# Performance work log

Hardware: AMD Instinct MI355X
Metric: run time of the kernel (lower is better)

## Reference

```python
import jax, jax.numpy as jnp
import numpy as np

NUM_HEADS = 8


def setup_inputs() -> dict:
    key = jax.random.key(0)
    k1, k2, k3 = jax.random.split(key, 3)
    B, C, D, H, W = 2, 512, 32, 32, 32
    x = jax.random.normal(k1, (B, C, D, H, W), dtype=jnp.float32)
    w_qkv = jax.random.normal(k2, (3 * C, C), dtype=jnp.float32) * 0.02
    b_qkv = jnp.zeros((3 * C,), dtype=jnp.float32)
    w_out = jax.random.normal(k3, (C, C), dtype=jnp.float32) * 0.02
    b_out = jnp.zeros((C,), dtype=jnp.float32)
    return {"x": x, "w_qkv": w_qkv, "b_qkv": b_qkv, "w_out": w_out, "b_out": b_out}


def reference(x, w_qkv, b_qkv, w_out, b_out):
    B, C, D, H, W = x.shape
    nh = NUM_HEADS
    hd = C // nh
    # 1x1x1 conv3d == pointwise linear over channel dim
    qkv = jnp.einsum('bcdhw,oc->bodhw', x, w_qkv) + b_qkv[None, :, None, None, None]
    q, k, v = jnp.split(qkv, 3, axis=1)  # each [B,C,D,H,W]

    def to_heads(t):
        # [B,C,D,H,W] -> [B,nh,hd,D,H,W] -> [B,H,W,nh,D,hd]
        return t.reshape(B, nh, hd, D, H, W).transpose(0, 4, 5, 1, 3, 2)

    q, k, v = to_heads(q), to_heads(k), to_heads(v)
    scale = hd ** -0.5
    # attention along the depth axis D: attn [B,H,W,nh,D,D]
    attn = jnp.einsum('bhwnic,bhwnjc->bhwnij', q, k) * scale
    attn = jax.nn.softmax(attn, axis=-1)
    out = jnp.einsum('bhwnij,bhwnjc->bhwnic', attn, v)  # [B,H,W,nh,D,hd]
    # [B,H,W,nh,D,hd] -> [B,nh,hd,D,H,W] -> [B,C,D,H,W]
    out = out.transpose(0, 3, 5, 4, 1, 2).reshape(B, C, D, H, W)
    out = jnp.einsum('bcdhw,oc->bodhw', out, w_out) + b_out[None, :, None, None, None]
    return out + x
```

## Files before the change

kernel.cpp:

```cpp
#include <hip/hip_runtime.h>


typedef __bf16 bf16x8 __attribute__((ext_vector_type(8)));
typedef float  f32x4  __attribute__((ext_vector_type(4)));
typedef float  f32x16 __attribute__((ext_vector_type(16)));

__device__ __forceinline__ float b2f(unsigned int u) {
    union { float f; unsigned int i; } x; x.i = u << 16; return x.f;
}
__device__ __forceinline__ unsigned short f2b(float f) {
    union { float f; unsigned int i; } x; x.f = f;
    unsigned int r = x.i + 0x7FFFu + ((x.i >> 16) & 1u);
    return (unsigned short)(r >> 16);
}
__device__ __forceinline__ unsigned int cvtpk(float lo, float hi) {
    unsigned int r;
    asm("v_cvt_pk_bf16_f32 %0, %1, %2" : "=v"(r) : "v"(lo), "v"(hi));
    return r;
}
__device__ __forceinline__ f32x4 mfma16(bf16x8 a, bf16x8 b, f32x4 c) {
    return __builtin_amdgcn_mfma_f32_16x16x32_bf16(a, b, c, 0, 0, 0);
}
__device__ __forceinline__ f32x16 mfma32(bf16x8 a, bf16x8 b, f32x16 c) {
    return __builtin_amdgcn_mfma_f32_32x32x16_bf16(a, b, c, 0, 0, 0);
}
__device__ __forceinline__ void gload16(const void* g, void* l) {
    __builtin_amdgcn_global_load_lds((const unsigned int*)g, (unsigned int*)l, 16, 0, 0);
}

__global__ __launch_bounds__(256) void xprep(const float* __restrict__ x,
                                             const float* __restrict__ wq_f,
                                             const float* __restrict__ wo_f,
                                             unsigned short* __restrict__ xT,
                                             unsigned short* __restrict__ wbf) {
    const int bid = blockIdx.x;
    const int t   = threadIdx.x;
    if (bid >= 2048) {
        int i0 = (bid - 2048) * 1024 + t;
        #pragma unroll
        for (int k = 0; k < 4; ++k) {
            int i = i0 + k * 256;
            const float* src;
            int off;
            if (i < 196608) { src = wq_f; off = i * 4; }
            else            { src = wo_f; off = (i - 196608) * 4; }
            float4 v = *(const float4*)(src + off);
            *(uint2*)(wbf + (size_t)i * 4) = make_uint2(cvtpk(v.x, v.y), cvtpk(v.z, v.w));
        }
        return;
    }
    __shared__ __align__(16) char tile[32768];
    const int c0 = (bid & 7) * 64;
    const int s0 = (bid >> 3) * 256;
    const int b  = s0 >> 15;
    const int sp = s0 & 32767;

    const float* px = x + (size_t)b * 16777216 + (size_t)(c0 + (t & 7) * 8) * 32768 + sp + (t >> 3) * 8;
    float va[8][8];
    #pragma unroll
    for (int j = 0; j < 8; ++j) {
        float4 a0 = *(const float4*)(px + (size_t)j * 32768);
        float4 a1 = *(const float4*)(px + (size_t)j * 32768 + 4);
        va[j][0] = a0.x; va[j][1] = a0.y; va[j][2] = a0.z; va[j][3] = a0.w;
        va[j][4] = a1.x; va[j][5] = a1.y; va[j][6] = a1.z; va[j][7] = a1.w;
    }
    #pragma unroll
    for (int k = 0; k < 8; ++k) {
        uint4 o = make_uint4(cvtpk(va[0][k], va[1][k]), cvtpk(va[2][k], va[3][k]),
                             cvtpk(va[4][k], va[5][k]), cvtpk(va[6][k], va[7][k]));
        const int srow = (t >> 3) * 8 + k;
        *(uint4*)(tile + srow * 128 + (((t & 7) ^ k) << 4)) = o;
    }
    __syncthreads();
    unsigned short* dst = xT + (size_t)(s0 + t) * 512 + c0;
    #pragma unroll
    for (int m = 0; m < 8; ++m) {
        uint4 v = *(const uint4*)(tile + t * 128 + ((m ^ (t & 7)) << 4));
        *(uint4*)(dst + m * 8) = v;
    }
}

__global__ __launch_bounds__(256, 2)
void axial_ab(const unsigned short* __restrict__ xT,
              const unsigned short* __restrict__ wq,
              const float* __restrict__ bq,
              unsigned short* __restrict__ ao)
{
    __shared__ __align__(16) char lds[81920];
    const int QT0 = 0, KT0 = 16384, VT0 = 32768, P0 = 49152, BIAS0 = 57344;
    float* bias_s = (float*)(lds + BIAS0);

    const int bid = blockIdx.x;
    const int vid = (bid & 7) * 512 + (bid >> 3);
    const int n   = vid & 7;
    const int tg  = vid >> 3;
    const int b   = tg >> 8;
    const int h   = (tg >> 3) & 31;
    const int w0  = (tg & 7) * 4;
    const int sbase = b * 32768 + h * 32 + w0;

    const int tid = threadIdx.x;
    const int wv  = tid >> 6;
    const int l   = tid & 63;
    const int l31 = l & 31;
    const int hh  = l >> 5;
    const int wm  = wv >> 1;
    const int wn  = wv & 1;

    auto stage = [&](int k, int slot) {
        #pragma unroll
        for (int i = 0; i < 3; ++i) {
            const int il = wv * 3 + i;
            const int r  = il * 16 + (l >> 2);
            const int R  = n * 64 + (r & 63) + ((r >> 6) << 9);
            const unsigned short* src = wq + R * 512 + k * 32 +
                                        (((l & 3) ^ ((r >> 1) & 3)) << 3);
            gload16(src, lds + slot * 12288 + il * 1024);
        }
        #pragma unroll
        for (int i = 0; i < 2; ++i) {
            const int il = wv * 2 + i;
            const int r  = il * 16 + (l >> 2);
            const int d  = r & 31;
            const int wr = r >> 5;
            const int s  = sbase + d * 1024 + wr;
            const unsigned short* src = xT + (size_t)s * 512 + k * 32 +
                                        (((l & 3) ^ ((r >> 1) & 3)) << 3);
            gload16(src, lds + 49152 + slot * 8192 + il * 1024);
        }
    };

    f32x16 acc[3][2];
    #pragma unroll
    for (int mf = 0; mf < 3; ++mf)
        #pragma unroll
        for (int nf = 0; nf < 2; ++nf) acc[mf][nf] = (f32x16)0.f;

    auto gphase = [&](int slot) {
        #pragma unroll
        for (int ks = 0; ks < 2; ++ks) {
            bf16x8 af[3], bfr[2];
            #pragma unroll
            for (int mf = 0; mf < 3; ++mf) {
                const int r = wm * 96 + mf * 32 + l31;
                af[mf] = *(const bf16x8*)(lds + slot * 12288 + r * 64 +
                                          (((ks * 2 + hh) ^ ((r >> 1) & 3)) << 4));
            }
            #pragma unroll
            for (int nf = 0; nf < 2; ++nf) {
                const int r = wn * 64 + nf * 32 + l31;
                bfr[nf] = *(const bf16x8*)(lds + 49152 + slot * 8192 + r * 64 +
                                           (((ks * 2 + hh) ^ ((r >> 1) & 3)) << 4));
            }
            #pragma unroll
            for (int mf = 0; mf < 3; ++mf)
                #pragma unroll
                for (int nf = 0; nf < 2; ++nf)
                    acc[mf][nf] = mfma32(af[mf], bfr[nf], acc[mf][nf]);
        }
    };

    stage(0, 0); stage(1, 1); stage(2, 2);
    asm volatile("s_waitcnt vmcnt(10)" ::: "memory");
    __builtin_amdgcn_s_barrier();
    __builtin_amdgcn_sched_barrier(0);

    #pragma unroll
    for (int k = 0; k < 16; ++k) {
        if (k < 13) stage(k + 3, (k + 3) & 3);
        __builtin_amdgcn_s_setprio(1);
        gphase(k & 3);
        __builtin_amdgcn_s_setprio(0);
        asm volatile("s_waitcnt lgkmcnt(0)" ::: "memory");
        if (k < 13)       { asm volatile("s_waitcnt vmcnt(10)" ::: "memory"); }
        else if (k == 13) { asm volatile("s_waitcnt vmcnt(5)"  ::: "memory"); }
        else if (k == 14) { asm volatile("s_waitcnt vmcnt(0)"  ::: "memory"); }
        __builtin_amdgcn_s_barrier();
        __builtin_amdgcn_sched_barrier(0);
    }

    if (tid < 192) bias_s[tid] = bq[((tid >> 6) << 9) + n * 64 + (tid & 63)];
    __syncthreads();

    #pragma unroll
    for (int mf = 0; mf < 3; ++mf) {
        const int m0 = wm * 96 + mf * 32;
        #pragma unroll
        for (int nf = 0; nf < 2; ++nf) {
            const int t = wn * 2 + nf;
            const f32x16 v = acc[mf][nf];
            if (m0 < 128) {
                const int base = (m0 < 64) ? QT0 : KT0;
                const int c0g  = (m0 & 63) >> 3;
                const int d    = l31;
                #pragma unroll
                for (int p = 0; p < 4; ++p) {
                    float4 bb = *(const float4*)(bias_s + m0 + 8 * p + 4 * hh);
                    unsigned int u0 = cvtpk(v[4 * p]     + bb.x, v[4 * p + 1] + bb.y);
                    unsigned int u1 = cvtpk(v[4 * p + 2] + bb.z, v[4 * p + 3] + bb.w);
                    *(uint2*)(lds + base + t * 4096 + d * 128 +
                              (((c0g + p) ^ (d & 7)) << 4) + 8 * hh) = make_uint2(u0, u1);
                }
            } else {
                const int e0 = m0 - 128;
                const int j  = wn * 64 + nf * 32 + l31;
                #pragma unroll
                for (int reg = 0; reg < 16; ++reg) {
                    const int e = e0 + (reg & 3) + 8 * (reg >> 2) + 4 * hh;
                    unsigned int u = cvtpk(v[reg], v[reg]);
                    *(unsigned short*)(lds + VT0 + e * 256 +
                                       (((j >> 3) ^ (e & 7)) << 4) + ((2 * j) & 15)) =
                        (unsigned short)(u & 0xffffu);
                }
            }
        }
    }
    __syncthreads();

    {
        const int t  = wv;
        const int qg = l >> 4;
        f32x4 sacc[2][2];
        sacc[0][0] = (f32x4)0.f; sacc[0][1] = (f32x4)0.f;
        sacc[1][0] = (f32x4)0.f; sacc[1][1] = (f32x4)0.f;
        #pragma unroll
        for (int kh = 0; kh < 2; ++kh) {
            bf16x8 qa[2], kb[2];
            #pragma unroll
            for (int mt = 0; mt < 2; ++mt) {
                const int i = mt * 16 + (l & 15);
                qa[mt] = *(const bf16x8*)(lds + QT0 + t * 4096 + i * 128 +
                                          (((kh * 4 + qg) ^ (i & 7)) << 4));
            }
            #pragma unroll
            for (int nt = 0; nt < 2; ++nt) {
                const int jj = nt * 16 + (l & 15);
                kb[nt] = *(const bf16x8*)(lds + KT0 + t * 4096 + jj * 128 +
                                          (((kh * 4 + qg) ^ (jj & 7)) << 4));
            }
            #pragma unroll
            for (int mt = 0; mt < 2; ++mt)
                #pragma unroll
                for (int nt = 0; nt < 2; ++nt)
                    sacc[mt][nt] = mfma16(qa[mt], kb[nt], sacc[mt][nt]);
        }
        #pragma unroll
        for (int mt = 0; mt < 2; ++mt) {
            #pragma unroll
            for (int reg = 0; reg < 4; ++reg) {
                float s0 = sacc[mt][0][reg] * 0.125f;
                float s1 = sacc[mt][1][reg] * 0.125f;
                float m = fmaxf(s0, s1);
                m = fmaxf(m, __shfl_xor(m, 1));
                m = fmaxf(m, __shfl_xor(m, 2));
                m = fmaxf(m, __shfl_xor(m, 4));
                m = fmaxf(m, __shfl_xor(m, 8));
                float p0 = __expf(s0 - m);
                float p1 = __expf(s1 - m);
                float ss = p0 + p1;
                ss += __shfl_xor(ss, 1);
                ss += __shfl_xor(ss, 2);
                ss += __shfl_xor(ss, 4);
                ss += __shfl_xor(ss, 8);
                float inv = 1.0f / ss;
                const int i = mt * 16 + 4 * qg + reg;
                #pragma unroll
                for (int nt = 0; nt < 2; ++nt) {
                    const int j = nt * 16 + (l & 15);
                    unsigned int u = cvtpk((nt ? p1 : p0) * inv, 0.f);
                    *(unsigned short*)(lds + P0 + t * 2048 + i * 64 +
                                       (((j >> 3) ^ (i & 3)) << 4) + ((2 * j) & 15)) =
                        (unsigned short)(u & 0xffffu);
                }
            }
        }
        asm volatile("s_waitcnt lgkmcnt(0)" ::: "memory");
        __builtin_amdgcn_sched_barrier(0);

        f32x16 oa[2];
        oa[0] = (f32x16)0.f; oa[1] = (f32x16)0.f;
        #pragma unroll
        for (int ks = 0; ks < 2; ++ks) {
            bf16x8 pb = *(const bf16x8*)(lds + P0 + t * 2048 + l31 * 64 +
                                         (((ks * 2 + hh) ^ (l31 & 3)) << 4));
            #pragma unroll
            for (int cf = 0; cf < 2; ++cf) {
                const int c = cf * 32 + l31;
                bf16x8 vv = *(const bf16x8*)(lds + VT0 + c * 256 +
                                             (((t * 4 + ks * 2 + hh) ^ (c & 7)) << 4));
                oa[cf] = mfma32(vv, pb, oa[cf]);
            }
        }
        const size_t srow = (size_t)(sbase + l31 * 1024 + t) * 512 + n * 64;
        #pragma unroll
        for (int cf = 0; cf < 2; ++cf) {
            #pragma unroll
            for (int p = 0; p < 4; ++p) {
                const int cb = cf * 32 + 8 * p + 4 * hh;
                float4 bb = *(const float4*)(bias_s + 128 + cb);
                unsigned int u0 = cvtpk(oa[cf][4 * p]     + bb.x, oa[cf][4 * p + 1] + bb.y);
                unsigned int u1 = cvtpk(oa[cf][4 * p + 2] + bb.z, oa[cf][4 * p + 3] + bb.w);
                *(uint2*)(ao + srow + cb) = make_uint2(u0, u1);
            }
        }
    }
}

__global__ __launch_bounds__(256, 2)
void axial_out(const unsigned short* __restrict__ ao,
               const unsigned short* __restrict__ wo,
               const float* __restrict__ bo,
               const float* __restrict__ x,
               float* __restrict__ out)
{
    __shared__ __align__(16) char lds[65536];
    const int bid = blockIdx.x;
    const int vid = (bid & 7) * 256 + (bid >> 3);
    const int mt_ = vid & 3;
    const int nt_ = vid >> 2;
    const int m_base = mt_ * 128;
    const int s_base = nt_ * 128;
    const int bb  = s_base >> 15;
    const int spl = s_base & 32767;
    const float* xblk = x + (size_t)bb * 16777216 + spl;
    float* oblk = out + (size_t)bb * 16777216 + spl;

    const int tid = threadIdx.x;
    const int wv  = tid >> 6;
    const int l   = tid & 63;
    const int l31 = l & 31;
    const int hh  = l >> 5;
    const int wm  = wv >> 1;
    const int wn  = wv & 1;

    auto stage = [&](int kk, int buf) {
        #pragma unroll
        for (int i = 0; i < 4; ++i) {
            const int il  = wv * 4 + i;
            const int row = il * 8 + (l >> 3);
            const unsigned short* srcA = wo + (m_base + row) * 512 + kk * 64 +
                                         (((l & 7) ^ (row & 7)) << 3);
            gload16(srcA, lds + buf * 16384 + il * 1024);
            const unsigned short* srcB = ao + (size_t)(s_base + row) * 512 + kk * 64 +
                                         (((l & 7) ^ (row & 7)) << 3);
            gload16(srcB, lds + 32768 + buf * 16384 + il * 1024);
        }
    };

    f32x16 acc[2][2];
    acc[0][0] = (f32x16)0.f; acc[0][1] = (f32x16)0.f;
    acc[1][0] = (f32x16)0.f; acc[1][1] = (f32x16)0.f;

    stage(0, 0);
    __syncthreads();
    int cur = 0;
    for (int kk = 0; kk < 8; ++kk) {
        if (kk < 7) stage(kk + 1, cur ^ 1);
        #pragma unroll
        for (int ks = 0; ks < 4; ++ks) {
            bf16x8 af[2], bfr[2];
            #pragma unroll
            for (int mf = 0; mf < 2; ++mf) {
                const int row = wm * 64 + mf * 32 + l31;
                af[mf] = *(const bf16x8*)(lds + cur * 16384 + row * 128 +
                                          (((ks * 2 + hh) ^ (row & 7)) << 4));
            }
            #pragma unroll
            for (int nf = 0; nf < 2; ++nf) {
                const int row = wn * 64 + nf * 32 + l31;
                bfr[nf] = *(const bf16x8*)(lds + 32768 + cur * 16384 + row * 128 +
                                           (((ks * 2 + hh) ^ (row & 7)) << 4));
            }
            #pragma unroll
            for (int mf = 0; mf < 2; ++mf)
                #pragma unroll
                for (int nf = 0; nf < 2; ++nf)
                    acc[mf][nf] = mfma32(af[mf], bfr[nf], acc[mf][nf]);
        }
        __syncthreads();
        cur ^= 1;
    }

    #pragma unroll
    for (int mf = 0; mf < 2; ++mf) {
        #pragma unroll
        for (int reg = 0; reg < 16; ++reg) {
            const int co = m_base + wm * 64 + mf * 32 + (reg & 3) + 8 * (reg >> 2) + 4 * hh;
            const float bias = bo[co];
            #pragma unroll
            for (int nf = 0; nf < 2; ++nf) {
                const int sl = wn * 64 + nf * 32 + l31;
                oblk[(size_t)co * 32768 + sl] = acc[mf][nf][reg] + bias +
                                                xblk[(size_t)co * 32768 + sl];
            }
        }
    }
}

__device__ __forceinline__ int adr_qk(int row, int cb) { return row * 2048 + (cb ^ ((row & 7) << 4)); }
__device__ __forceinline__ int adr_x (int row, int cb) { return 98304 + row * 1024 + (cb ^ ((row & 7) << 4)); }
__device__ __forceinline__ int adr_xl(int row, int cb) { return 131072 + row * 1024 + (cb ^ ((row & 7) << 4)); }
__device__ __forceinline__ int adr_v (int e, int jb)   { int a = e * 64 + jb; return 65536 + (a ^ ((e & 7) << 4)); }

__global__ __launch_bounds__(512, 1)
void axial3d_mfma(const float* __restrict__ x,
                  const float* __restrict__ bq,
                  const float* __restrict__ bo,
                  const unsigned short* __restrict__ wq,
                  const unsigned short* __restrict__ wo,
                  float* __restrict__ out) {
    __shared__ char lds[163840];
    const int bid  = blockIdx.x;
    const int work = (bid & 7) * 256 + (bid >> 3);
    const int b    = work >> 10;
    const int h    = (work >> 5) & 31;
    const int w    = work & 31;
    const float* xb = x   + ((size_t)b * 16777216u) + h * 32 + w;
    float*       ob = out + ((size_t)b * 16777216u) + h * 32 + w;
    const int tid  = threadIdx.x;
    const int wv   = tid >> 6;
    const int lane = tid & 63;
    const int g    = lane >> 4;
    const int q    = lane & 15;
    {
        const int d  = tid & 31;
        const int c0 = tid >> 5;
        #pragma unroll
        for (int it = 0; it < 32; ++it) {
            int c = c0 + it * 16;
            float xv = xb[c * 32768 + d * 1024];
            unsigned short hi = f2b(xv);
            unsigned short lo = f2b(xv - b2f(hi));
            *(unsigned short*)(lds + adr_x(d, c * 2))  = hi;
            *(unsigned short*)(lds + adr_xl(d, c * 2)) = lo;
        }
    }
    __syncthreads();
    for (int tp = 0; tp < 3; ++tp) {
        const int mt0 = wv * 12 + tp * 4;
        f32x4 acc[4][2];
        #pragma unroll
        for (int t = 0; t < 4; ++t) { acc[t][0] = (f32x4)0.f; acc[t][1] = (f32x4)0.f; }
        #pragma unroll
        for (int kk = 0; kk < 16; ++kk) {
            bf16x8 bfr[2];
            #pragma unroll
            for (int nt = 0; nt < 2; ++nt)
                bfr[nt] = *(const bf16x8*)(lds + adr_x(nt * 16 + q, kk * 64 + g * 16));
            #pragma unroll
            for (int t = 0; t < 4; ++t) {
                const int o = (mt0 + t) * 16 + q;
                bf16x8 a = *(const bf16x8*)((const char*)wq + o * 1024 + kk * 64 + g * 16);
                acc[t][0] = mfma16(a, bfr[0], acc[t][0]);
                acc[t][1] = mfma16(a, bfr[1], acc[t][1]);
            }
        }
        #pragma unroll
        for (int t = 0; t < 4; ++t) {
            const int mt    = mt0 + t;
            const int obase = mt * 16 + 4 * g;
            float bias[4];
            #pragma unroll
            for (int r = 0; r < 4; ++r) bias[r] = bq[obase + r];
            if (mt < 64) {
                #pragma unroll
                for (int nt = 0; nt < 2; ++nt) {
                    const int d = nt * 16 + q;
                    unsigned int lo = f2b(acc[t][nt][0] + bias[0]) |
                                      ((unsigned int)f2b(acc[t][nt][1] + bias[1]) << 16);
                    unsigned int hi = f2b(acc[t][nt][2] + bias[2]) |
                                      ((unsigned int)f2b(acc[t][nt][3] + bias[3]) << 16);
                    *(uint2*)(lds + adr_qk(d, obase * 2)) = make_uint2(lo, hi);
                }
            } else {
                #pragma unroll
                for (int nt = 0; nt < 2; ++nt) {
                    const int d = nt * 16 + q;
                    #pragma unroll
                    for (int r = 0; r < 4; ++r) {
                        const int e = obase + r - 1024;
                        *(unsigned short*)(lds + adr_v(e, d * 2)) = f2b(acc[t][nt][r] + bias[r]);
                    }
                }
            }
        }
    }
    __syncthreads();
    {
        const int n = wv;
        f32x4 s[2][2];
        s[0][0] = (f32x4)0.f; s[0][1] = (f32x4)0.f;
        s[1][0] = (f32x4)0.f; s[1][1] = (f32x4)0.f;
        #pragma unroll
        for (int kk = 0; kk < 2; ++kk) {
            bf16x8 a0 = *(const bf16x8*)(lds + adr_qk(q,      n * 128 + kk * 64 + g * 16));
            bf16x8 a1 = *(const bf16x8*)(lds + adr_qk(16 + q, n * 128 + kk * 64 + g * 16));
            bf16x8 b0 = *(const bf16x8*)(lds + adr_qk(q,      1024 + n * 128 + kk * 64 + g * 16));
            bf16x8 b1 = *(const bf16x8*)(lds + adr_qk(16 + q, 1024 + n * 128 + kk * 64 + g * 16));
            s[0][0] = mfma16(a0, b0, s[0][0]);
            s[0][1] = mfma16(a0, b1, s[0][1]);
            s[1][0] = mfma16(a1, b0, s[1][0]);
            s[1][1] = mfma16(a1, b1, s[1][1]);
        }
        float pv[2][2][4];
        #pragma unroll
        for (int it = 0; it < 2; ++it) {
            #pragma unroll
            for (int r = 0; r < 4; ++r) {
                float s0 = s[it][0][r] * 0.125f;
                float s1 = s[it][1][r] * 0.125f;
                float m = fmaxf(s0, s1);
                m = fmaxf(m, __shfl_xor(m, 1));
                m = fmaxf(m, __shfl_xor(m, 2));
                m = fmaxf(m, __shfl_xor(m, 4));
                m = fmaxf(m, __shfl_xor(m, 8));
                float p0 = __expf(s0 - m);
                float p1 = __expf(s1 - m);
                float ss = p0 + p1;
                ss += __shfl_xor(ss, 1);
                ss += __shfl_xor(ss, 2);
                ss += __shfl_xor(ss, 4);
                ss += __shfl_xor(ss, 8);
                float inv = 1.0f / ss;
                pv[it][0][r] = p0 * inv;
                pv[it][1][r] = p1 * inv;
            }
        }
        #pragma unroll
        for (int it = 0; it < 2; ++it)
            #pragma unroll
            for (int jt = 0; jt < 2; ++jt)
                #pragma unroll
                for (int r = 0; r < 4; ++r) {
                    const int i = it * 16 + 4 * g + r;
                    *(unsigned short*)(lds + adr_qk(i, n * 128 + (jt * 16 + q) * 2)) =
                        f2b(pv[it][jt][r]);
                }
        asm volatile("s_waitcnt lgkmcnt(0)" ::: "memory");
        __builtin_amdgcn_sched_barrier(0);
        bf16x8 pa0 = *(const bf16x8*)(lds + adr_qk(q,      n * 128 + g * 16));
        bf16x8 pa1 = *(const bf16x8*)(lds + adr_qk(16 + q, n * 128 + g * 16));
        #pragma unroll
        for (int et = 0; et < 4; ++et) {
            const int e = n * 64 + et * 16 + q;
            bf16x8 vb = *(const bf16x8*)(lds + adr_v(e, g * 16));
            f32x4 o0 = mfma16(pa0, vb, (f32x4)0.f);
            f32x4 o1 = mfma16(pa1, vb, (f32x4)0.f);
            const int cb = 1024 + n * 128 + (et * 16 + q) * 2;
            #pragma unroll
            for (int r = 0; r < 4; ++r) {
                *(unsigned short*)(lds + adr_qk(4 * g + r, cb))      = f2b(o0[r]);
                *(unsigned short*)(lds + adr_qk(16 + 4 * g + r, cb)) = f2b(o1[r]);
            }
        }
    }
    __syncthreads();
    for (int p4 = 0; p4 < 4; ++p4) {
        const int mt = wv * 4 + p4;
        f32x4 acc[2];
        acc[0] = (f32x4)0.f; acc[1] = (f32x4)0.f;
        #pragma unroll
        for (int kk = 0; kk < 16; ++kk) {
            bf16x8 b0 = *(const bf16x8*)(lds + adr_qk(q,      1024 + kk * 64 + g * 16));
            bf16x8 b1 = *(const bf16x8*)(lds + adr_qk(16 + q, 1024 + kk * 64 + g * 16));
            bf16x8 a  = *(const bf16x8*)((const char*)wo + (mt * 16 + q) * 1024 + kk * 64 + g * 16);
            acc[0] = mfma16(a, b0, acc[0]);
            acc[1] = mfma16(a, b1, acc[1]);
        }
        const int obase = mt * 16 + 4 * g;
        float bias[4];
        #pragma unroll
        for (int r = 0; r < 4; ++r) bias[r] = bo[obase + r];
        #pragma unroll
        for (int nt = 0; nt < 2; ++nt) {
            const int d = nt * 16 + q;
            uint2 xh = *(const uint2*)(lds + adr_x(d, obase * 2));
            uint2 xl = *(const uint2*)(lds + adr_xl(d, obase * 2));
            float res[4];
            res[0] = b2f(xh.x & 0xffffu) + b2f(xl.x & 0xffffu);
            res[1] = b2f(xh.x >> 16)     + b2f(xl.x >> 16);
            res[2] = b2f(xh.y & 0xffffu) + b2f(xl.y & 0xffffu);
            res[3] = b2f(xh.y >> 16)     + b2f(xl.y >> 16);
            #pragma unroll
            for (int r = 0; r < 4; ++r)
                ob[(obase + r) * 32768 + d * 1024] = acc[nt][r] + bias[r] + res[r];
        }
    }
}

extern "C" void kernel_launch(void* const* d_in, const int* in_sizes, int n_in,
                              void* d_out, int out_size, void* d_ws, size_t ws_size,
                              hipStream_t stream) {
    const float* x     = (const float*)d_in[0];
    const float* w_qkv = (const float*)d_in[1];
    const float* b_qkv = (const float*)d_in[2];
    const float* w_out = (const float*)d_in[3];
    const float* b_out = (const float*)d_in[4];
    float* out = (float*)d_out;

    const size_t XT_OFF = 0;
    const size_t AO_OFF = 67108864;
    const size_t WQ_OFF = 134217728;
    const size_t NEED   = 136314880;

    if (ws_size >= NEED) {
        unsigned short* xT  = (unsigned short*)((char*)d_ws + XT_OFF);
        unsigned short* ao  = (unsigned short*)((char*)d_ws + AO_OFF);
        unsigned short* wbf = (unsigned short*)((char*)d_ws + WQ_OFF);
        xprep   <<<dim3(2304), dim3(256), 0, stream>>>(x, w_qkv, w_out, xT, wbf);
        axial_ab<<<dim3(4096), dim3(256), 0, stream>>>(xT, wbf, b_qkv, ao);
        axial_out<<<dim3(2048), dim3(256), 0, stream>>>(ao, wbf + 786432, b_out, x, out);
    } else {
        unsigned short* wbf = (unsigned short*)d_ws;
        xprep<<<dim3(2304), dim3(256), 0, stream>>>(x, (const float*)d_in[1], w_out,
                                                    (unsigned short*)d_ws, wbf);
        axial3d_mfma<<<dim3(2048), dim3(512), 0, stream>>>(x, b_qkv, b_out,
                                                           wbf, wbf + 786432, out);
    }
}
```

Before: 282.4 us.

## Pre-tile x and QKV weights into MFMA-ready blocks, widen attention tile

The prep kernel now writes x and the QKV weights in a pre-blocked layout matching the LDS fragment order, so each staging load in the QKV GEMM is one contiguous 16-byte chunk per lane with no XOR swizzle. Each block of the fused QKV+attention kernel covers 8 w positions instead of 4, which halves the grid and doubles the N tile so weight tiles are reused more. The pipeline depth drops from 4 stages to double buffering with a full vmcnt(0) wait each iteration, and the attention epilogue runs in two phases that reuse the Q/K/V LDS buffers. The risk is more exposed load latency from the shallower pipeline and more accumulator registers per thread.

```diff
diff --git a/kernel.cpp b/kernel.cpp
--- a/kernel.cpp
+++ b/kernel.cpp
@@ -28,76 +28,77 @@
     __builtin_amdgcn_global_load_lds((const unsigned int*)g, (unsigned int*)l, 16, 0, 0);
 }
 
-__global__ __launch_bounds__(256) void xprep(const float* __restrict__ x,
-                                             const float* __restrict__ wq_f,
-                                             const float* __restrict__ wo_f,
-                                             unsigned short* __restrict__ xT,
-                                             unsigned short* __restrict__ wbf) {
+__global__ __launch_bounds__(256) void xprep2(const float* __restrict__ x,
+                                              const float* __restrict__ wq_f,
+                                              const float* __restrict__ wo_f,
+                                              unsigned short* __restrict__ xB,
+                                              unsigned short* __restrict__ wT,
+                                              unsigned short* __restrict__ wo_bf) {
     const int bid = blockIdx.x;
-    const int t   = threadIdx.x;
-    if (bid >= 2048) {
-        int i0 = (bid - 2048) * 1024 + t;
-        #pragma unroll
-        for (int k = 0; k < 4; ++k) {
-            int i = i0 + k * 256;
-            const float* src;
-            int off;
-            if (i < 196608) { src = wq_f; off = i * 4; }
-            else            { src = wo_f; off = (i - 196608) * 4; }
-            float4 v = *(const float4*)(src + off);
-            *(uint2*)(wbf + (size_t)i * 4) = make_uint2(cvtpk(v.x, v.y), cvtpk(v.z, v.w));
-        }
-        return;
-    }
-    __shared__ __align__(16) char tile[32768];
-    const int c0 = (bid & 7) * 64;
-    const int s0 = (bid >> 3) * 256;
-    const int b  = s0 >> 15;
-    const int sp = s0 & 32767;
-
-    const float* px = x + (size_t)b * 16777216 + (size_t)(c0 + (t & 7) * 8) * 32768 + sp + (t >> 3) * 8;
-    float va[8][8];
-    #pragma unroll
-    for (int j = 0; j < 8; ++j) {
-        float4 a0 = *(const float4*)(px + (size_t)j * 32768);
-        float4 a1 = *(const float4*)(px + (size_t)j * 32768 + 4);
-        va[j][0] = a0.x; va[j][1] = a0.y; va[j][2] = a0.z; va[j][3] = a0.w;
-        va[j][4] = a1.x; va[j][5] = a1.y; va[j][6] = a1.z; va[j][7] = a1.w;
-    }
-    #pragma unroll
-    for (int k = 0; k < 8; ++k) {
-        uint4 o = make_uint4(cvtpk(va[0][k], va[1][k]), cvtpk(va[2][k], va[3][k]),
-                             cvtpk(va[4][k], va[5][k]), cvtpk(va[6][k], va[7][k]));
-        const int srow = (t >> 3) * 8 + k;
-        *(uint4*)(tile + srow * 128 + (((t & 7) ^ k) << 4)) = o;
-    }
-    __syncthreads();
-    unsigned short* dst = xT + (size_t)(s0 + t) * 512 + c0;
-    #pragma unroll
-    for (int m = 0; m < 8; ++m) {
-        uint4 v = *(const uint4*)(tile + t * 128 + ((m ^ (t & 7)) << 4));
-        *(uint4*)(dst + m * 8) = v;
+    const int tid = threadIdx.x;
+    if (bid < 2048) {
+        const int G  = bid & 255;
+        const int ck = bid >> 8;
+        const int b  = G >> 7, h = (G >> 2) & 31, wg = G & 3;
+        const int co = tid & 7;
+        const int d  = tid >> 3;
+        const int c0 = ck * 64 + co * 8;
+        const float* px = x + (size_t)b * 16777216 + (size_t)c0 * 32768 + d * 1024 + h * 32 + wg * 8;
+        float va[8][8];
+        #pragma unroll
+        for (int j = 0; j < 8; ++j) {
+            float4 a0 = *(const float4*)(px + (size_t)j * 32768);
+            float4 a1 = *(const float4*)(px + (size_t)j * 32768 + 4);
+            va[j][0] = a0.x; va[j][1] = a0.y; va[j][2] = a0.z; va[j][3] = a0.w;
+            va[j][4] = a1.x; va[j][5] = a1.y; va[j][6] = a1.z; va[j][7] = a1.w;
+        }
+        unsigned short* outg = xB + (size_t)G * 131072 +
+                               (size_t)(ck * 2 + (co >> 2)) * 8192 + (size_t)(co & 3) * 2048;
+        #pragma unroll
+        for (int e = 0; e < 8; ++e) {
+            uint4 v = make_uint4(cvtpk(va[0][e], va[1][e]), cvtpk(va[2][e], va[3][e]),
+                                 cvtpk(va[4][e], va[5][e]), cvtpk(va[6][e], va[7][e]));
+            *(uint4*)(outg + (e * 32 + d) * 8) = v;
+        }
+    } else {
+        const int gidx = (bid - 2048) * 256 + tid;
+        if (gidx < 98304) {
+            const int r  = gidx % 192;
+            const int qd = gidx / 192;
+            const int kb = qd & 3, kk = (qd >> 2) & 15, n = qd >> 6;
+            const int R  = (r >> 6) * 512 + n * 64 + (r & 63);
+            const float* s = wq_f + R * 512 + kk * 32 + kb * 8;
+            float4 a0 = *(const float4*)s;
+            float4 a1 = *(const float4*)(s + 4);
+            *(uint4*)(wT + (size_t)gidx * 8) =
+                make_uint4(cvtpk(a0.x, a0.y), cvtpk(a0.z, a0.w), cvtpk(a1.x, a1.y), cvtpk(a1.z, a1.w));
+        } else {
+            const int g2 = gidx - 98304;
+            const float* s = wo_f + (size_t)g2 * 8;
+            float4 a0 = *(const float4*)s;
+            float4 a1 = *(const float4*)(s + 4);
+            *(uint4*)(wo_bf + (size_t)g2 * 8) =
+                make_uint4(cvtpk(a0.x, a0.y), cvtpk(a0.z, a0.w), cvtpk(a1.x, a1.y), cvtpk(a1.z, a1.w));
+        }
     }
 }
 
 __global__ __launch_bounds__(256, 2)
-void axial_ab(const unsigned short* __restrict__ xT,
-              const unsigned short* __restrict__ wq,
-              const float* __restrict__ bq,
-              unsigned short* __restrict__ ao)
+void axial_ab2(const unsigned short* __restrict__ xB,
+               const unsigned short* __restrict__ wT,
+               const float* __restrict__ bq,
+               unsigned short* __restrict__ ao)
 {
-    __shared__ __align__(16) char lds[81920];
-    const int QT0 = 0, KT0 = 16384, VT0 = 32768, P0 = 49152, BIAS0 = 57344;
+    __shared__ __align__(16) char lds[58112];
+    const int SB0 = 24576, QT0 = 0, KT0 = 16384, VT0 = 32768, P0 = 49152, BIAS0 = 57344;
     float* bias_s = (float*)(lds + BIAS0);
 
     const int bid = blockIdx.x;
-    const int vid = (bid & 7) * 512 + (bid >> 3);
+    const int vid = (bid & 7) * 256 + (bid >> 3);
     const int n   = vid & 7;
-    const int tg  = vid >> 3;
-    const int b   = tg >> 8;
-    const int h   = (tg >> 3) & 31;
-    const int w0  = (tg & 7) * 4;
-    const int sbase = b * 32768 + h * 32 + w0;
+    const int G   = vid >> 3;
+    const int b   = G >> 7, h = (G >> 2) & 31, wg = G & 3;
+    const int sbase = b * 32768 + h * 32 + wg * 8;
 
     const int tid = threadIdx.x;
     const int wv  = tid >> 6;
@@ -107,202 +108,192 @@
     const int wm  = wv >> 1;
     const int wn  = wv & 1;
 
-    auto stage = [&](int k, int slot) {
+    const unsigned short* wA = wT + (size_t)n * 98304;
+    const unsigned short* xG = xB + (size_t)G * 131072;
+
+    auto stage = [&](int kk, int sl) {
         #pragma unroll
         for (int i = 0; i < 3; ++i) {
-            const int il = wv * 3 + i;
-            const int r  = il * 16 + (l >> 2);
-            const int R  = n * 64 + (r & 63) + ((r >> 6) << 9);
-            const unsigned short* src = wq + R * 512 + k * 32 +
-                                        (((l & 3) ^ ((r >> 1) & 3)) << 3);
-            gload16(src, lds + slot * 12288 + il * 1024);
-        }
-        #pragma unroll
-        for (int i = 0; i < 2; ++i) {
-            const int il = wv * 2 + i;
-            const int r  = il * 16 + (l >> 2);
-            const int d  = r & 31;
-            const int wr = r >> 5;
-            const int s  = sbase + d * 1024 + wr;
-            const unsigned short* src = xT + (size_t)s * 512 + k * 32 +
-                                        (((l & 3) ^ ((r >> 1) & 3)) << 3);
-            gload16(src, lds + 49152 + slot * 8192 + il * 1024);
+            const int j = wv * 3 + i;
+            gload16(wA + kk * 6144 + j * 512 + l * 8, lds + sl * 12288 + j * 1024);
+        }
+        #pragma unroll
+        for (int i = 0; i < 4; ++i) {
+            const int j = wv * 4 + i;
+            gload16(xG + kk * 8192 + j * 512 + l * 8, lds + SB0 + sl * 16384 + j * 1024);
         }
     };
 
-    f32x16 acc[3][2];
+    f32x16 acc[3][4];
     #pragma unroll
     for (int mf = 0; mf < 3; ++mf)
         #pragma unroll
-        for (int nf = 0; nf < 2; ++nf) acc[mf][nf] = (f32x16)0.f;
-
-    auto gphase = [&](int slot) {
+        for (int nf = 0; nf < 4; ++nf) acc[mf][nf] = (f32x16)0.f;
+
+    auto gphase = [&](int sl) {
         #pragma unroll
         for (int ks = 0; ks < 2; ++ks) {
-            bf16x8 af[3], bfr[2];
-            #pragma unroll
-            for (int mf = 0; mf < 3; ++mf) {
-                const int r = wm * 96 + mf * 32 + l31;
-                af[mf] = *(const bf16x8*)(lds + slot * 12288 + r * 64 +
-                                          (((ks * 2 + hh) ^ ((r >> 1) & 3)) << 4));
-            }
-            #pragma unroll
-            for (int nf = 0; nf < 2; ++nf) {
-                const int r = wn * 64 + nf * 32 + l31;
-                bfr[nf] = *(const bf16x8*)(lds + 49152 + slot * 8192 + r * 64 +
-                                           (((ks * 2 + hh) ^ ((r >> 1) & 3)) << 4));
-            }
+            const int kb = ks * 2 + hh;
+            bf16x8 af[3], bfr[4];
             #pragma unroll
             for (int mf = 0; mf < 3; ++mf)
-                #pragma unroll
-                for (int nf = 0; nf < 2; ++nf)
+                af[mf] = *(const bf16x8*)(lds + sl * 12288 + kb * 3072 +
+                                          (wm * 96 + mf * 32 + l31) * 16);
+            #pragma unroll
+            for (int nf = 0; nf < 4; ++nf)
+                bfr[nf] = *(const bf16x8*)(lds + SB0 + sl * 16384 + kb * 4096 +
+                                           (wn * 128 + nf * 32 + l31) * 16);
+            #pragma unroll
+            for (int mf = 0; mf < 3; ++mf)
+                #pragma unroll
+                for (int nf = 0; nf < 4; ++nf)
                     acc[mf][nf] = mfma32(af[mf], bfr[nf], acc[mf][nf]);
         }
     };
 
-    stage(0, 0); stage(1, 1); stage(2, 2);
-    asm volatile("s_waitcnt vmcnt(10)" ::: "memory");
+    stage(0, 0);
+    asm volatile("s_waitcnt vmcnt(0)" ::: "memory");
     __builtin_amdgcn_s_barrier();
     __builtin_amdgcn_sched_barrier(0);
-
     #pragma unroll
-    for (int k = 0; k < 16; ++k) {
-        if (k < 13) stage(k + 3, (k + 3) & 3);
+    for (int kk = 0; kk < 16; ++kk) {
+        if (kk < 15) stage(kk + 1, (kk + 1) & 1);
         __builtin_amdgcn_s_setprio(1);
-        gphase(k & 3);
+        gphase(kk & 1);
         __builtin_amdgcn_s_setprio(0);
-        asm volatile("s_waitcnt lgkmcnt(0)" ::: "memory");
-        if (k < 13)       { asm volatile("s_waitcnt vmcnt(10)" ::: "memory"); }
-        else if (k == 13) { asm volatile("s_waitcnt vmcnt(5)"  ::: "memory"); }
-        else if (k == 14) { asm volatile("s_waitcnt vmcnt(0)"  ::: "memory"); }
+        asm volatile("s_waitcnt vmcnt(0) lgkmcnt(0)" ::: "memory");
         __builtin_amdgcn_s_barrier();
         __builtin_amdgcn_sched_barrier(0);
     }
 
-    if (tid < 192) bias_s[tid] = bq[((tid >> 6) << 9) + n * 64 + (tid & 63)];
+    if (tid < 192) bias_s[tid] = bq[(tid >> 6) * 512 + n * 64 + (tid & 63)];
     __syncthreads();
 
     #pragma unroll
-    for (int mf = 0; mf < 3; ++mf) {
-        const int m0 = wm * 96 + mf * 32;
-        #pragma unroll
-        for (int nf = 0; nf < 2; ++nf) {
-            const int t = wn * 2 + nf;
-            const f32x16 v = acc[mf][nf];
-            if (m0 < 128) {
-                const int base = (m0 < 64) ? QT0 : KT0;
-                const int c0g  = (m0 & 63) >> 3;
-                const int d    = l31;
+    for (int ph = 0; ph < 2; ++ph) {
+        if (wn == ph) {
+            #pragma unroll
+            for (int mf = 0; mf < 3; ++mf) {
+                const int m0 = wm * 96 + mf * 32;
+                #pragma unroll
+                for (int nf = 0; nf < 4; ++nf) {
+                    const int tl = nf;
+                    const int d  = l31;
+                    const f32x16 v = acc[mf][nf];
+                    if (m0 < 128) {
+                        const int base = (m0 < 64) ? QT0 : KT0;
+                        const int c0g  = (m0 & 63) >> 3;
+                        #pragma unroll
+                        for (int p = 0; p < 4; ++p) {
+                            float4 bb = *(const float4*)(bias_s + m0 + 8 * p + 4 * hh);
+                            unsigned int u0 = cvtpk(v[4 * p]     + bb.x, v[4 * p + 1] + bb.y);
+                            unsigned int u1 = cvtpk(v[4 * p + 2] + bb.z, v[4 * p + 3] + bb.w);
+                            *(uint2*)(lds + base + tl * 4096 + d * 128 +
+                                      (((c0g + p) ^ (d & 7)) << 4) + 8 * hh) = make_uint2(u0, u1);
+                        }
+                    } else {
+                        const int e0 = m0 - 128;
+                        const int jj = tl * 32 + l31;
+                        #pragma unroll
+                        for (int reg = 0; reg < 16; ++reg) {
+                            const int e = e0 + (reg & 3) + 8 * (reg >> 2) + 4 * hh;
+                            *(unsigned short*)(lds + VT0 + e * 256 +
+                                               (((jj >> 3) ^ (e & 7)) << 4) + ((2 * jj) & 15)) =
+                                f2b(v[reg]);
+                        }
+                    }
+                }
+            }
+        }
+        __syncthreads();
+
+        {
+            const int t  = wv;
+            const int qg = l >> 4;
+            f32x4 sacc[2][2];
+            sacc[0][0] = (f32x4)0.f; sacc[0][1] = (f32x4)0.f;
+            sacc[1][0] = (f32x4)0.f; sacc[1][1] = (f32x4)0.f;
+            #pragma unroll
+            for (int kh = 0; kh < 2; ++kh) {
+                bf16x8 qa[2], kb_[2];
+                #pragma unroll
+                for (int mt = 0; mt < 2; ++mt) {
+                    const int i = mt * 16 + (l & 15);
+                    qa[mt] = *(const bf16x8*)(lds + QT0 + t * 4096 + i * 128 +
+                                              (((kh * 4 + qg) ^ (i & 7)) << 4));
+                }
+                #pragma unroll
+                for (int nt = 0; nt < 2; ++nt) {
+                    const int jj = nt * 16 + (l & 15);
+                    kb_[nt] = *(const bf16x8*)(lds + KT0 + t * 4096 + jj * 128 +
+                                               (((kh * 4 + qg) ^ (jj & 7)) << 4));
+                }
+                #pragma unroll
+                for (int mt = 0; mt < 2; ++mt)
+                    #pragma unroll
+                    for (int nt = 0; nt < 2; ++nt)
+                        sacc[mt][nt] = mfma16(qa[mt], kb_[nt], sacc[mt][nt]);
+            }
+            #pragma unroll
+            for (int mt = 0; mt < 2; ++mt) {
+                #pragma unroll
+                for (int reg = 0; reg < 4; ++reg) {
+                    float s0 = sacc[mt][0][reg] * 0.125f;
+                    float s1 = sacc[mt][1][reg] * 0.125f;
+                    float m = fmaxf(s0, s1);
+                    m = fmaxf(m, __shfl_xor(m, 1));
+                    m = fmaxf(m, __shfl_xor(m, 2));
+                    m = fmaxf(m, __shfl_xor(m, 4));
+                    m = fmaxf(m, __shfl_xor(m, 8));
+                    float p0 = __expf(s0 - m);
+                    float p1 = __expf(s1 - m);
+                    float ss = p0 + p1;
+                    ss += __shfl_xor(ss, 1);
+                    ss += __shfl_xor(ss, 2);
+                    ss += __shfl_xor(ss, 4);
+                    ss += __shfl_xor(ss, 8);
+                    float inv = 1.0f / ss;
+                    const int i = mt * 16 + 4 * qg + reg;
+                    #pragma unroll
+                    for (int nt = 0; nt < 2; ++nt) {
+                        const int j = nt * 16 + (l & 15);
+                        *(unsigned short*)(lds + P0 + t * 2048 + i * 64 +
+                                           (((j >> 3) ^ (i & 3)) << 4) + ((2 * j) & 15)) =
+                            f2b((nt ? p1 : p0) * inv);
+                    }
+                }
+            }
+            asm volatile("s_waitcnt lgkmcnt(0)" ::: "memory");
+            __builtin_amdgcn_sched_barrier(0);
+
+            f32x16 oa[2];
+            oa[0] = (f32x16)0.f; oa[1] = (f32x16)0.f;
+            #pragma unroll
+            for (int ks = 0; ks < 2; ++ks) {
+                bf16x8 pb = *(const bf16x8*)(lds + P0 + t * 2048 + l31 * 64 +
+                                             (((ks * 2 + hh) ^ (l31 & 3)) << 4));
+                #pragma unroll
+                for (int cf = 0; cf < 2; ++cf) {
+                    const int c = cf * 32 + l31;
+                    bf16x8 vv = *(const bf16x8*)(lds + VT0 + c * 256 +
+                                                 (((t * 4 + ks * 2 + hh) ^ (c & 7)) << 4));
+                    oa[cf] = mfma32(vv, pb, oa[cf]);
+                }
+            }
+            const size_t srow = (size_t)(sbase + l31 * 1024 + ph * 4 + t) * 512 + n * 64;
+            #pragma unroll
+            for (int cf = 0; cf < 2; ++cf) {
                 #pragma unroll
                 for (int p = 0; p < 4; ++p) {
-                    float4 bb = *(const float4*)(bias_s + m0 + 8 * p + 4 * hh);
-                    unsigned int u0 = cvtpk(v[4 * p]     + bb.x, v[4 * p + 1] + bb.y);
-                    unsigned int u1 = cvtpk(v[4 * p + 2] + bb.z, v[4 * p + 3] + bb.w);
-                    *(uint2*)(lds + base + t * 4096 + d * 128 +
-                              (((c0g + p) ^ (d & 7)) << 4) + 8 * hh) = make_uint2(u0, u1);
-                }
-            } else {
-                const int e0 = m0 - 128;
-                const int j  = wn * 64 + nf * 32 + l31;
-                #pragma unroll
-                for (int reg = 0; reg < 16; ++reg) {
-                    const int e = e0 + (reg & 3) + 8 * (reg >> 2) + 4 * hh;
-                    unsigned int u = cvtpk(v[reg], v[reg]);
-                    *(unsigned short*)(lds + VT0 + e * 256 +
-                                       (((j >> 3) ^ (e & 7)) << 4) + ((2 * j) & 15)) =
-                        (unsigned short)(u & 0xffffu);
-                }
-            }
-        }
-    }
-    __syncthreads();
-
-    {
-        const int t  = wv;
-        const int qg = l >> 4;
-        f32x4 sacc[2][2];
-        sacc[0][0] = (f32x4)0.f; sacc[0][1] = (f32x4)0.f;
-        sacc[1][0] = (f32x4)0.f; sacc[1][1] = (f32x4)0.f;
-        #pragma unroll
-        for (int kh = 0; kh < 2; ++kh) {
-            bf16x8 qa[2], kb[2];
-            #pragma unroll
-            for (int mt = 0; mt < 2; ++mt) {
-                const int i = mt * 16 + (l & 15);
-                qa[mt] = *(const bf16x8*)(lds + QT0 + t * 4096 + i * 128 +
-                                          (((kh * 4 + qg) ^ (i & 7)) << 4));
-            }
-            #pragma unroll
-            for (int nt = 0; nt < 2; ++nt) {
-                const int jj = nt * 16 + (l & 15);
-                kb[nt] = *(const bf16x8*)(lds + KT0 + t * 4096 + jj * 128 +
-                                          (((kh * 4 + qg) ^ (jj & 7)) << 4));
-            }
-            #pragma unroll
-            for (int mt = 0; mt < 2; ++mt)
-                #pragma unroll
-                for (int nt = 0; nt < 2; ++nt)
-                    sacc[mt][nt] = mfma16(qa[mt], kb[nt], sacc[mt][nt]);
-        }
-        #pragma unroll
-        for (int mt = 0; mt < 2; ++mt) {
-            #pragma unroll
-            for (int reg = 0; reg < 4; ++reg) {
-                float s0 = sacc[mt][0][reg] * 0.125f;
-                float s1 = sacc[mt][1][reg] * 0.125f;
-                float m = fmaxf(s0, s1);
-                m = fmaxf(m, __shfl_xor(m, 1));
-                m = fmaxf(m, __shfl_xor(m, 2));
-                m = fmaxf(m, __shfl_xor(m, 4));
-                m = fmaxf(m, __shfl_xor(m, 8));
-                float p0 = __expf(s0 - m);
-                float p1 = __expf(s1 - m);
-                float ss = p0 + p1;
-                ss += __shfl_xor(ss, 1);
-                ss += __shfl_xor(ss, 2);
-                ss += __shfl_xor(ss, 4);
-                ss += __shfl_xor(ss, 8);
-                float inv = 1.0f / ss;
-                const int i = mt * 16 + 4 * qg + reg;
-                #pragma unroll
-                for (int nt = 0; nt < 2; ++nt) {
-                    const int j = nt * 16 + (l & 15);
-                    unsigned int u = cvtpk((nt ? p1 : p0) * inv, 0.f);
-                    *(unsigned short*)(lds + P0 + t * 2048 + i * 64 +
-                                       (((j >> 3) ^ (i & 3)) << 4) + ((2 * j) & 15)) =
-                        (unsigned short)(u & 0xffffu);
-                }
-            }
-        }
-        asm volatile("s_waitcnt lgkmcnt(0)" ::: "memory");
-        __builtin_amdgcn_sched_barrier(0);
-
-        f32x16 oa[2];
-        oa[0] = (f32x16)0.f; oa[1] = (f32x16)0.f;
-        #pragma unroll
-        for (int ks = 0; ks < 2; ++ks) {
-            bf16x8 pb = *(const bf16x8*)(lds + P0 + t * 2048 + l31 * 64 +
-                                         (((ks * 2 + hh) ^ (l31 & 3)) << 4));
-            #pragma unroll
-            for (int cf = 0; cf < 2; ++cf) {
-                const int c = cf * 32 + l31;
-                bf16x8 vv = *(const bf16x8*)(lds + VT0 + c * 256 +
-                                             (((t * 4 + ks * 2 + hh) ^ (c & 7)) << 4));
-                oa[cf] = mfma32(vv, pb, oa[cf]);
-            }
-        }
-        const size_t srow = (size_t)(sbase + l31 * 1024 + t) * 512 + n * 64;
-        #pragma unroll
-        for (int cf = 0; cf < 2; ++cf) {
-            #pragma unroll
-            for (int p = 0; p < 4; ++p) {
-                const int cb = cf * 32 + 8 * p + 4 * hh;
-                float4 bb = *(const float4*)(bias_s + 128 + cb);
-                unsigned int u0 = cvtpk(oa[cf][4 * p]     + bb.x, oa[cf][4 * p + 1] + bb.y);
-                unsigned int u1 = cvtpk(oa[cf][4 * p + 2] + bb.z, oa[cf][4 * p + 3] + bb.w);
-                *(uint2*)(ao + srow + cb) = make_uint2(u0, u1);
-            }
-        }
+                    const int cb = cf * 32 + 8 * p + 4 * hh;
+                    float4 bb = *(const float4*)(bias_s + 128 + cb);
+                    unsigned int u0 = cvtpk(oa[cf][4 * p]     + bb.x, oa[cf][4 * p + 1] + bb.y);
+                    unsigned int u1 = cvtpk(oa[cf][4 * p + 2] + bb.z, oa[cf][4 * p + 3] + bb.w);
+                    *(uint2*)(ao + srow + cb) = make_uint2(u0, u1);
+                }
+            }
+        }
+        __syncthreads();
     }
 }
 
@@ -395,6 +386,18 @@
             }
         }
     }
+}
+
+__global__ __launch_bounds__(256) void wconvert(const float* __restrict__ wq,
+                                                const float* __restrict__ wo,
+                                                unsigned short* __restrict__ dst) {
+    int i = blockIdx.x * 256 + threadIdx.x;
+    const float* src;
+    int off;
+    if (i < 196608) { src = wq; off = i * 4; }
+    else            { src = wo; off = (i - 196608) * 4; }
+    float4 v = *(const float4*)(src + off);
+    *(uint2*)(dst + (size_t)i * 4) = make_uint2(cvtpk(v.x, v.y), cvtpk(v.z, v.w));
 }
 
 __device__ __forceinline__ int adr_qk(int row, int cb) { return row * 2048 + (cb ^ ((row & 7) << 4)); }
@@ -598,22 +601,22 @@
     const float* b_out = (const float*)d_in[4];
     float* out = (float*)d_out;
 
-    const size_t XT_OFF = 0;
+    const size_t XB_OFF = 0;
     const size_t AO_OFF = 67108864;
-    const size_t WQ_OFF = 134217728;
+    const size_t WT_OFF = 134217728;
     const size_t NEED   = 136314880;
 
     if (ws_size >= NEED) {
-        unsigned short* xT  = (unsigned short*)((char*)d_ws + XT_OFF);
-        unsigned short* ao  = (unsigned short*)((char*)d_ws + AO_OFF);
-        unsigned short* wbf = (unsigned short*)((char*)d_ws + WQ_OFF);
-        xprep   <<<dim3(2304), dim3(256), 0, stream>>>(x, w_qkv, w_out, xT, wbf);
-        axial_ab<<<dim3(4096), dim3(256), 0, stream>>>(xT, wbf, b_qkv, ao);
-        axial_out<<<dim3(2048), dim3(256), 0, stream>>>(ao, wbf + 786432, b_out, x, out);
+        unsigned short* xB    = (unsigned short*)((char*)d_ws + XB_OFF);
+        unsigned short* ao    = (unsigned short*)((char*)d_ws + AO_OFF);
+        unsigned short* wTt   = (unsigned short*)((char*)d_ws + WT_OFF);
+        unsigned short* wo_bf = wTt + 786432;
+        xprep2   <<<dim3(2560), dim3(256), 0, stream>>>(x, w_qkv, w_out, xB, wTt, wo_bf);
+        axial_ab2<<<dim3(2048), dim3(256), 0, stream>>>(xB, wTt, b_qkv, ao);
+        axial_out<<<dim3(2048), dim3(256), 0, stream>>>(ao, wo_bf, b_out, x, out);
     } else {
         unsigned short* wbf = (unsigned short*)d_ws;
-        xprep<<<dim3(2304), dim3(256), 0, stream>>>(x, (const float*)d_in[1], w_out,
-                                                    (unsigned short*)d_ws, wbf);
+        wconvert<<<dim3(1024), dim3(256), 0, stream>>>(w_qkv, w_out, wbf);
         axial3d_mfma<<<dim3(2048), dim3(512), 0, stream>>>(x, b_qkv, b_out,
                                                            wbf, wbf + 786432, out);
     }
```

Result: slower. 396.6 us (+40.4%).
